# Kernel optimization log

Measured on AMD Instinct MI355X. Metric: run time of the kernel, lower is better.

Reference implementation:

```python
import jax, jax.numpy as jnp
import numpy as np

Q, C, T = 256, 128, 128
L = Q + C + T            # 512
D = 1024                 # d_model
H = 8                    # heads
DK = D // H              # 128 = self_attn.d_k
F = 3                    # num_latent_relations
R = 50                   # num_relation_kinds = len(relations2id)
FF = 4 * D               # feed-forward hidden
DEFAULT_QQ_ID = 0        # relations2id['q:q-default']
EPS = 1e-5


def setup_inputs():
    key = jax.random.key(0)
    ks = jax.random.split(key, 40)
    s = 0.02
    def nrm(k, shape, scale=s):
        return jax.random.normal(k, shape, jnp.float32) * scale
    inp = {
        'x': jax.random.normal(ks[0], (1, L, D), jnp.float32),
        'qc_relation': jax.random.uniform(ks[1], (Q, C, F), jnp.float32),
        'cq_relation': jax.random.uniform(ks[2], (C, Q, F), jnp.float32),
        'qt_relation': jax.random.uniform(ks[3], (Q, T, F), jnp.float32),
        'tq_relation': jax.random.uniform(ks[4], (T, Q, F), jnp.float32),
        'ct_relation': jax.random.randint(ks[5], (C + T, C + T), 0, R, jnp.int32),
        'predefined_relation': jax.random.randint(ks[6], (L, L), 0, R, jnp.int32),
        'mask': jnp.ones((1, L, L), jnp.int32),
        # relation embedding tables
        'rel_k_emb': nrm(ks[7], (R, DK)), 'rel_v_emb': nrm(ks[8], (R, DK)),
        'lqc_k': nrm(ks[9], (F, DK)), 'lqc_v': nrm(ks[10], (F, DK)),
        'lcq_k': nrm(ks[11], (F, DK)), 'lcq_v': nrm(ks[12], (F, DK)),
        'lqt_k': nrm(ks[13], (F, DK)), 'lqt_v': nrm(ks[14], (F, DK)),
        'ltq_k': nrm(ks[15], (F, DK)), 'ltq_v': nrm(ks[16], (F, DK)),
        # attention projections (torch Linear: y = x @ W.T + b)
        'Wq': nrm(ks[17], (D, D)), 'bq': jnp.zeros((D,), jnp.float32),
        'Wk': nrm(ks[18], (D, D)), 'bk': jnp.zeros((D,), jnp.float32),
        'Wv': nrm(ks[19], (D, D)), 'bv': jnp.zeros((D,), jnp.float32),
        'Wo': nrm(ks[20], (D, D)), 'bo': jnp.zeros((D,), jnp.float32),
        # layer norms
        'ln1_g': jnp.ones((D,), jnp.float32), 'ln1_b': jnp.zeros((D,), jnp.float32),
        'ln2_g': jnp.ones((D,), jnp.float32), 'ln2_b': jnp.zeros((D,), jnp.float32),
        # FFN
        'W1': nrm(ks[21], (FF, D)), 'b1': jnp.zeros((FF,), jnp.float32),
        'W2': nrm(ks[22], (D, FF)), 'b2': jnp.zeros((D,), jnp.float32),
    }
    return inp


def layer_norm(x, g, b):
    m = jnp.mean(x, -1, keepdims=True)
    v = jnp.mean((x - m) ** 2, -1, keepdims=True)
    return (x - m) * jax.lax.rsqrt(v + EPS) * g + b


def build_latent_relation(ct, qc, cq, qt, tq, emb, lqc, lcq, lqt, ltq):
    # qq block: every entry is the default-qq embedding row
    qq = jnp.broadcast_to(emb[DEFAULT_QQ_ID], (Q, Q, DK))
    qc_e = jnp.einsum('qcf,fd->qcd', qc, lqc)
    cq_e = jnp.einsum('cqf,fd->cqd', cq, lcq)
    qt_e = jnp.einsum('qtf,fd->qtd', qt, lqt)
    tq_e = jnp.einsum('tqf,fd->tqd', tq, ltq)
    ct_e = emb[ct]                                      # [(c+t),(c+t),DK]
    top = jnp.concatenate([qq, qc_e, qt_e], axis=1)      # [Q, L, DK]
    bot = jnp.concatenate([jnp.concatenate([cq_e, tq_e], 0), ct_e], axis=1)  # [C+T, L, DK]
    return jnp.concatenate([top, bot], axis=0)           # [L, L, DK]


def relation_attention(x, rel_k, rel_v, mask, Wq, bq, Wk, bk, Wv, bv, Wo, bo):
    B = x.shape[0]
    def proj(W, b):
        return (x @ W.T + b).reshape(B, L, H, DK).transpose(0, 2, 1, 3)  # [B,H,L,DK]
    q, k, v = proj(Wq, bq), proj(Wk, bk), proj(Wv, bv)
    scores = (jnp.einsum('bhid,bhjd->bhij', q, k)
              + jnp.einsum('bhid,ijd->bhij', q, rel_k)) / jnp.sqrt(jnp.float32(DK))
    scores = jnp.where(mask[:, None] == 0, jnp.float32(-1e9), scores)
    p = jax.nn.softmax(scores, axis=-1)
    o = (jnp.einsum('bhij,bhjd->bhid', p, v)
         + jnp.einsum('bhij,ijd->bhid', p, rel_v))
    o = o.transpose(0, 2, 1, 3).reshape(B, L, D)
    return o @ Wo.T + bo


def reference(x, qc_relation, cq_relation, qt_relation, tq_relation,
              ct_relation, predefined_relation, mask,
              rel_k_emb, rel_v_emb, lqc_k, lqc_v, lcq_k, lcq_v,
              lqt_k, lqt_v, ltq_k, ltq_v,
              Wq, bq, Wk, bk, Wv, bv, Wo, bo,
              ln1_g, ln1_b, ln2_g, ln2_b, W1, b1, W2, b2):
    # latent relation build + combine with predefined lookup
    rel_k = (rel_k_emb[predefined_relation]
             + build_latent_relation(ct_relation, qc_relation, cq_relation,
                                     qt_relation, tq_relation,
                                     rel_k_emb, lqc_k, lcq_k, lqt_k, ltq_k))
    rel_v = (rel_v_emb[predefined_relation]
             + build_latent_relation(ct_relation, qc_relation, cq_relation,
                                     qt_relation, tq_relation,
                                     rel_v_emb, lqc_v, lcq_v, lqt_v, ltq_v))
    # sublayer 0: pre-norm relation-biased self attention (dropout=0)
    h = x + relation_attention(layer_norm(x, ln1_g, ln1_b), rel_k, rel_v, mask,
                               Wq, bq, Wk, bk, Wv, bv, Wo, bo)
    # sublayer 1: pre-norm FFN
    y = layer_norm(h, ln2_g, ln2_b)
    ffn = jax.nn.relu(y @ W1.T + b1) @ W2.T + b2
    return h + ffn
```

## Files before the change

### kernel.cpp

```cpp
#include <hip/hip_runtime.h>
#include <hip/hip_bf16.h>

#define LL 512
#define DD 1024
#define HH 8
#define DKK 128
#define QQ 256
#define CCC 128
#define TTT 128
#define RR 50
#define FFF 4096
#define KLD 576
#define SLD 576

typedef __attribute__((ext_vector_type(8))) short short8;
typedef __attribute__((ext_vector_type(4))) float float4v;

__device__ __forceinline__ unsigned short f2bu(float f) {
  __hip_bfloat16 h = __float2bfloat16(f);
  unsigned short u; __builtin_memcpy(&u, &h, 2); return u;
}
__device__ __forceinline__ float b2f(unsigned short u) {
  unsigned int v = ((unsigned int)u) << 16;
  float f; __builtin_memcpy(&f, &v, 4); return f;
}
__device__ __forceinline__ int4 cvt8(float4 x, float4 y) {
  int4 o;
  o.x = (int)f2bu(x.x) | ((int)f2bu(x.y) << 16);
  o.y = (int)f2bu(x.z) | ((int)f2bu(x.w) << 16);
  o.z = (int)f2bu(y.x) | ((int)f2bu(y.y) << 16);
  o.w = (int)f2bu(y.z) | ((int)f2bu(y.w) << 16);
  return o;
}

__device__ __forceinline__ void lds_barrier() {
  __builtin_amdgcn_sched_barrier(0);
  __builtin_amdgcn_s_waitcnt(0xC07F);
  __builtin_amdgcn_s_barrier();
  __builtin_amdgcn_sched_barrier(0);
}

#define LOADSET(A0,A1,B0,B1,F0,F1,F2,F3,itv) { int k0v = (itv) << 6;          \
  A0 = *(const int4*)(Az + (size_t)(bm + r)*lda + k0v + gc*8);                \
  A1 = *(const int4*)(Az + (size_t)(bm + 32 + r)*lda + k0v + gc*8);           \
  if constexpr (!CONVB) {                                                     \
    B0 = *(const int4*)(Bz16 + (size_t)(bnb + r)*ldb + k0v + gc*8);           \
    if constexpr (NB > 1)                                                     \
      B1 = *(const int4*)(Bz16 + (size_t)(bnb + 32 + r)*ldb + k0v + gc*8);    \
  } else {                                                                    \
    F0 = *(const float4*)(Bz32 + (size_t)(bnb + r)*ldb + k0v + gc*8);         \
    F1 = *(const float4*)(Bz32 + (size_t)(bnb + r)*ldb + k0v + gc*8 + 4);     \
    if constexpr (NB > 1) {                                                   \
      F2 = *(const float4*)(Bz32 + (size_t)(bnb + 32 + r)*ldb + k0v + gc*8);  \
      F3 = *(const float4*)(Bz32 + (size_t)(bnb + 32 + r)*ldb + k0v + gc*8 + 4); } } }

#define STORESET2(basep,A0,A1,B0,B1,F0,F1,F2,F3) {                            \
  char* bse = (basep);                                                        \
  *(int4*)(bse + r*128 + sl*16) = A0;                                         \
  *(int4*)(bse + (32 + r)*128 + sl*16) = A1;                                  \
  if constexpr (!CONVB) {                                                     \
    *(int4*)(bse + ABYTES + r*128 + sl*16) = B0;                              \
    if constexpr (NB > 1)                                                     \
      *(int4*)(bse + ABYTES + (32 + r)*128 + sl*16) = B1;                     \
  } else {                                                                    \
    *(int4*)(bse + ABYTES + r*128 + sl*16) = cvt8(F0, F1);                    \
    if constexpr (NB > 1)                                                     \
      *(int4*)(bse + ABYTES + (32 + r)*128 + sl*16) = cvt8(F2, F3); } }

__global__ __launch_bounds__(256) void kprep_kernel(
    const float* __restrict__ embk,
    const float* __restrict__ lqc, const float* __restrict__ lqt,
    const float* __restrict__ lcq, const float* __restrict__ ltq,
    unsigned short* __restrict__ Kh)
{
  int g = blockIdx.x*256 + threadIdx.x;
  if (g >= 8*64*128) return;
  int d = g & 127, rr = (g >> 7) & 63, h = g >> 13;
  float v = 0.f;
  if (rr < 50) v = embk[rr*128 + d];
  else if (rr < 62) {
    int u = rr - 50; int tb = u/3, f = u - tb*3;
    const float* tab = (tb==0) ? lqc : (tb==1) ? lqt : (tb==2) ? lcq : ltq;
    v = tab[f*128 + d];
  }
  Kh[((size_t)h*KLD + 512 + rr)*DKK + d] = f2bu(v);
}

__global__ __launch_bounds__(256) void ln_bf16_kernel(const float* __restrict__ x,
    const float* __restrict__ g, const float* __restrict__ b,
    unsigned short* __restrict__ y)
{
  int row = blockIdx.x, t = threadIdx.x;
  const float4 xv = ((const float4*)(x + row*DD))[t];
  float s  = xv.x+xv.y+xv.z+xv.w;
  float ss = xv.x*xv.x+xv.y*xv.y+xv.z*xv.z+xv.w*xv.w;
  __shared__ float rs[256], rss[256];
  rs[t]=s; rss[t]=ss; __syncthreads();
  for (int st=128; st>0; st>>=1){ if (t<st){ rs[t]+=rs[t+st]; rss[t]+=rss[t+st]; } __syncthreads(); }
  float mean = rs[0] * (1.0f/DD);
  float var  = rss[0]*(1.0f/DD) - mean*mean;
  float inv  = rsqrtf(var + 1e-5f);
  float4 gv = ((const float4*)g)[t], bv = ((const float4*)b)[t];
  ushort4 ov;
  ov.x = f2bu((xv.x-mean)*inv*gv.x + bv.x);
  ov.y = f2bu((xv.y-mean)*inv*gv.y + bv.y);
  ov.z = f2bu((xv.z-mean)*inv*gv.z + bv.z);
  ov.w = f2bu((xv.w-mean)*inv*gv.w + bv.w);
  ((ushort4*)(y + row*DD))[t] = ov;
}

__global__ __launch_bounds__(256) void ln_bf16_addb_kernel(float* __restrict__ x,
    const float* __restrict__ g, const float* __restrict__ b,
    const float* __restrict__ b2, unsigned short* __restrict__ y)
{
  int row = blockIdx.x, t = threadIdx.x;
  const float4 xv = ((const float4*)(x + row*DD))[t];
  float s  = xv.x+xv.y+xv.z+xv.w;
  float ss = xv.x*xv.x+xv.y*xv.y+xv.z*xv.z+xv.w*xv.w;
  __shared__ float rs[256], rss[256];
  rs[t]=s; rss[t]=ss; __syncthreads();
  for (int st=128; st>0; st>>=1){ if (t<st){ rs[t]+=rs[t+st]; rss[t]+=rss[t+st]; } __syncthreads(); }
  float mean = rs[0] * (1.0f/DD);
  float var  = rss[0]*(1.0f/DD) - mean*mean;
  float inv  = rsqrtf(var + 1e-5f);
  float4 gv = ((const float4*)g)[t], bv = ((const float4*)b)[t];
  ushort4 ov;
  ov.x = f2bu((xv.x-mean)*inv*gv.x + bv.x);
  ov.y = f2bu((xv.y-mean)*inv*gv.y + bv.y);
  ov.z = f2bu((xv.z-mean)*inv*gv.z + bv.z);
  ov.w = f2bu((xv.w-mean)*inv*gv.w + bv.w);
  ((ushort4*)(y + row*DD))[t] = ov;
  float4 b2v = ((const float4*)b2)[t];
  float4 nx; nx.x = xv.x+b2v.x; nx.y = xv.y+b2v.y; nx.z = xv.z+b2v.z; nx.w = xv.w+b2v.w;
  ((float4*)(x + row*DD))[t] = nx;
}

template<int BN, int DEPTH, int CONVB, int ZK, int OUT_BF16, int RELU, int HAS_SRC, int HAS_BIAS>
__global__ __launch_bounds__(256) void gemm_pl(
    const unsigned short* __restrict__ A, int lda, size_t sAz,
    const void* __restrict__ Bv, int ldb, size_t sBz,
    const float* __restrict__ bias,
    const float* __restrict__ src, int ldsrc, size_t sSz,
    void* __restrict__ Cv, int ldc, size_t sCz,
    int K)
{
  constexpr int BM = 64;
  constexpr int WM = 32, WN = BN/2, FM = 2, FN = WN/16;
  constexpr int NB = BN/32;
  constexpr int ABYTES = BM*128, TILE = ABYTES + BN*128;
  __shared__ char lds[2*TILE];
  int t = threadIdx.x, w = t >> 6, l = t & 63;
  size_t z = blockIdx.z;
  const unsigned short* Az = A + z*sAz;
  const unsigned short* Bz16 = (const unsigned short*)Bv + (CONVB ? 0 : z*sBz);
  const float*          Bz32 = (const float*)Bv + (CONVB ? z*sBz : 0);
  int bm = blockIdx.y*BM, bn = blockIdx.x*BN;
  int bnb = bn;
  int wm = (w>>1)*WM, wn = (w&1)*WN;

  float4v acc[FM][FN];
  #pragma unroll
  for (int m=0;m<FM;++m)
    #pragma unroll
    for (int n=0;n<FN;++n) acc[m][n] = (float4v){0.f,0.f,0.f,0.f};

  int r = t >> 3, sl = t & 7;
  int gc = sl ^ (r & 7);
  int quad = l >> 4, lrow = l & 15;
  const int nit = K >> 6;

  int4 Aa0, Aa1, Ab0, Ab1;  float4 Af0, Af1, Af2, Af3;
  int4 Ba0, Ba1, Bb0, Bb1;  float4 Bf0, Bf1, Bf2, Bf3;
  int4 Ca0, Ca1, Cb0, Cb1;  float4 Cf0, Cf1, Cf2, Cf3;
  int4 Da0, Da1, Db0, Db1;  float4 Df0, Df1, Df2, Df3;

  auto compute = [&](const char* base) {
    const char* ab = base;
    const char* bb = base + ABYTES;
    #pragma unroll
    for (int step=0; step<2; ++step) {
      int c = step*4 + quad;
      short8 af[FM], bf[FN];
      #pragma unroll
      for (int m=0;m<FM;++m) {
        int Rw = wm + m*16 + lrow;
        af[m] = *(const short8*)(ab + Rw*128 + ((c ^ (Rw & 7))*16));
      }
      #pragma unroll
      for (int n=0;n<FN;++n) {
        int Rw = wn + n*16 + lrow;
        bf[n] = *(const short8*)(bb + Rw*128 + ((c ^ (Rw & 7))*16));
      }
      #pragma unroll
      for (int m=0;m<FM;++m)
        #pragma unroll
        for (int n=0;n<FN;++n)
          acc[m][n] = __builtin_amdgcn_mfma_f32_16x16x32_bf16(af[m], bf[n], acc[m][n], 0, 0, 0);
    }
  };

  if constexpr (DEPTH == 2) {
    LOADSET(Aa0,Aa1,Ab0,Ab1,Af0,Af1,Af2,Af3, 0);
    LOADSET(Ba0,Ba1,Bb0,Bb1,Bf0,Bf1,Bf2,Bf3, 1);
    for (int it = 0; it < nit; it += 2) {
      STORESET2(lds, Aa0,Aa1,Ab0,Ab1,Af0,Af1,Af2,Af3);
      if (it + 2 < nit) LOADSET(Aa0,Aa1,Ab0,Ab1,Af0,Af1,Af2,Af3, it+2);
      lds_barrier();
      compute(lds);
      STORESET2(lds + TILE, Ba0,Ba1,Bb0,Bb1,Bf0,Bf1,Bf2,Bf3);
      if (it + 3 < nit) LOADSET(Ba0,Ba1,Bb0,Bb1,Bf0,Bf1,Bf2,Bf3, it+3);
      lds_barrier();
      compute(lds + TILE);
    }
  } else {
    LOADSET(Aa0,Aa1,Ab0,Ab1,Af0,Af1,Af2,Af3, 0);
    LOADSET(Ba0,Ba1,Bb0,Bb1,Bf0,Bf1,Bf2,Bf3, 1);
    LOADSET(Ca0,Ca1,Cb0,Cb1,Cf0,Cf1,Cf2,Cf3, 2);
    LOADSET(Da0,Da1,Db0,Db1,Df0,Df1,Df2,Df3, 3);
    for (int it = 0; it < nit; it += 4) {
      STORESET2(lds, Aa0,Aa1,Ab0,Ab1,Af0,Af1,Af2,Af3);
      if (it + 4 < nit) LOADSET(Aa0,Aa1,Ab0,Ab1,Af0,Af1,Af2,Af3, it+4);
      lds_barrier();
      compute(lds);
      STORESET2(lds + TILE, Ba0,Ba1,Bb0,Bb1,Bf0,Bf1,Bf2,Bf3);
      if (it + 5 < nit) LOADSET(Ba0,Ba1,Bb0,Bb1,Bf0,Bf1,Bf2,Bf3, it+5);
      lds_barrier();
      compute(lds + TILE);
      STORESET2(lds, Ca0,Ca1,Cb0,Cb1,Cf0,Cf1,Cf2,Cf3);
      if (it + 6 < nit) LOADSET(Ca0,Ca1,Cb0,Cb1,Cf0,Cf1,Cf2,Cf3, it+6);
      lds_barrier();
      compute(lds);
      STORESET2(lds + TILE, Da0,Da1,Db0,Db1,Df0,Df1,Df2,Df3);
      if (it + 7 < nit) LOADSET(Da0,Da1,Db0,Db1,Df0,Df1,Df2,Df3, it+7);
      lds_barrier();
      compute(lds + TILE);
    }
  }

  #pragma unroll
  for (int m=0;m<FM;++m)
    #pragma unroll
    for (int n=0;n<FN;++n)
      #pragma unroll
      for (int rg=0;rg<4;++rg) {
        int row = bm + wm + m*16 + quad*4 + rg;
        int col = bn + wn + n*16 + lrow;
        float vv = acc[m][n][rg];
        if (ZK) {
          atomicAdd(&((float*)Cv)[(size_t)row*ldc + col], vv);
        } else {
          if (HAS_BIAS) vv += bias[col];
          if (HAS_SRC)  vv += src[z*sSz + (size_t)row*ldsrc + col];
          if (RELU) vv = fmaxf(vv, 0.f);
          if (OUT_BF16) ((unsigned short*)Cv)[z*sCz + (size_t)row*ldc + col] = f2bu(vv);
          else          ((float*)Cv)[z*sCz + (size_t)row*ldc + col] = vv;
        }
      }
}

__global__ __launch_bounds__(256) void gemm_qkv_pl(
    const unsigned short* __restrict__ A,
    const float* __restrict__ Wq, const float* __restrict__ Wk,
    const float* __restrict__ Wv,
    const float* __restrict__ bq, const float* __restrict__ bk,
    const float* __restrict__ bv,
    unsigned short* __restrict__ Qh, unsigned short* __restrict__ Kh,
    unsigned short* __restrict__ Vt)
{
  constexpr int BN = 64, CONVB = 1;
  constexpr int WM = 32, WN = 32, FM = 2, FN = 2;
  constexpr int NB = 2;
  constexpr int ABYTES = 64*128, TILE = ABYTES + BN*128;
  __shared__ char lds[2*TILE];
  int t = threadIdx.x, w = t >> 6, l = t & 63;
  int bm = blockIdx.y*64, bn = blockIdx.x*BN;
  int wm = (w>>1)*WM, wn = (w&1)*WN;
  const int lda = DD, ldb = DD, nit = DD >> 6;
  const unsigned short* Az = A;
  int part0 = bn >> 10;
  const float* Bz32 = (part0==0 ? Wq : part0==1 ? Wk : Wv) + (size_t)(bn & 1023)*DD;
  const unsigned short* Bz16 = nullptr; (void)Bz16;
  int bnb = 0;

  float4v acc[FM][FN];
  #pragma unroll
  for (int m=0;m<FM;++m)
    #pragma unroll
    for (int n=0;n<FN;++n) acc[m][n] = (float4v){0.f,0.f,0.f,0.f};

  int r = t >> 3, sl = t & 7;
  int gc = sl ^ (r & 7);
  int quad = l >> 4, lrow = l & 15;

  int4 Aa0, Aa1, Ab0, Ab1;  float4 Af0, Af1, Af2, Af3;
  int4 Ba0, Ba1, Bb0, Bb1;  float4 Bf0, Bf1, Bf2, Bf3;
  int4 Ca0, Ca1, Cb0, Cb1;  float4 Cf0, Cf1, Cf2, Cf3;
  int4 Da0, Da1, Db0, Db1;  float4 Df0, Df1, Df2, Df3;

  auto compute = [&](const char* base) {
    const char* ab = base;
    const char* bb = base + ABYTES;
    #pragma unroll
    for (int step=0; step<2; ++step) {
      int c = step*4 + quad;
      short8 af[FM], bf[FN];
      #pragma unroll
      for (int m=0;m<FM;++m) {
        int Rw = wm + m*16 + lrow;
        af[m] = *(const short8*)(ab + Rw*128 + ((c ^ (Rw & 7))*16));
      }
      #pragma unroll
      for (int n=0;n<FN;++n) {
        int Rw = wn + n*16 + lrow;
        bf[n] = *(const short8*)(bb + Rw*128 + ((c ^ (Rw & 7))*16));
      }
      #pragma unroll
      for (int m=0;m<FM;++m)
        #pragma unroll
        for (int n=0;n<FN;++n)
          acc[m][n] = __builtin_amdgcn_mfma_f32_16x16x32_bf16(af[m], bf[n], acc[m][n], 0, 0, 0);
    }
  };

  LOADSET(Aa0,Aa1,Ab0,Ab1,Af0,Af1,Af2,Af3, 0);
  LOADSET(Ba0,Ba1,Bb0,Bb1,Bf0,Bf1,Bf2,Bf3, 1);
  LOADSET(Ca0,Ca1,Cb0,Cb1,Cf0,Cf1,Cf2,Cf3, 2);
  LOADSET(Da0,Da1,Db0,Db1,Df0,Df1,Df2,Df3, 3);
  for (int it = 0; it < nit; it += 4) {
    STORESET2(lds, Aa0,Aa1,Ab0,Ab1,Af0,Af1,Af2,Af3);
    if (it + 4 < nit) LOADSET(Aa0,Aa1,Ab0,Ab1,Af0,Af1,Af2,Af3, it+4);
    lds_barrier();
    compute(lds);
    STORESET2(lds + TILE, Ba0,Ba1,Bb0,Bb1,Bf0,Bf1,Bf2,Bf3);
    if (it + 5 < nit) LOADSET(Ba0,Ba1,Bb0,Bb1,Bf0,Bf1,Bf2,Bf3, it+5);
    lds_barrier();
    compute(lds + TILE);
    STORESET2(lds, Ca0,Ca1,Cb0,Cb1,Cf0,Cf1,Cf2,Cf3);
    if (it + 6 < nit) LOADSET(Ca0,Ca1,Cb0,Cb1,Cf0,Cf1,Cf2,Cf3, it+6);
    lds_barrier();
    compute(lds);
    STORESET2(lds + TILE, Da0,Da1,Db0,Db1,Df0,Df1,Df2,Df3);
    if (it + 7 < nit) LOADSET(Da0,Da1,Db0,Db1,Df0,Df1,Df2,Df3, it+7);
    lds_barrier();
    compute(lds + TILE);
  }

  #pragma unroll
  for (int m=0;m<FM;++m)
    #pragma unroll
    for (int n=0;n<FN;++n)
      #pragma unroll
      for (int rg=0;rg<4;++rg) {
        int row = bm + wm + m*16 + quad*4 + rg;
        int col = bn + wn + n*16 + lrow;
        int part = col >> 10, hh = (col >> 7) & 7, d = col & 127;
        const float* bp = (part==0) ? bq : (part==1) ? bk : bv;
        float vv = acc[m][n][rg] + bp[col & 1023];
        unsigned short o = f2bu(vv);
        if (part == 0)      Qh[((size_t)hh*LL + row)*DKK + d] = o;
        else if (part == 1) Kh[((size_t)hh*KLD + row)*DKK + d] = o;
        else                Vt[((size_t)hh*DKK + d)*LL + row] = o;
      }
}

#define AT_QROWB 272
#define AT_KROWB 272
#define AT_SROW  584
#define AT_PROWB 1040
#define AT_VROWB 144
#define AT_OFF_KT 4352
#define AT_OFF_S  21760
#define AT_OFF_V  21760
#define AT_OFF_PW 59136
#define AT_OFF_PF1 62464
#define AT_OFF_PF2 62720
#define AT_LDS 62976

__global__ __launch_bounds__(256) void attn_fused(
    const unsigned short* __restrict__ Qh, const unsigned short* __restrict__ Kh,
    const unsigned short* __restrict__ Vt,
    const float* __restrict__ qcr, const float* __restrict__ cqr,
    const float* __restrict__ qtr, const float* __restrict__ tqr,
    const int* __restrict__ ct, const int* __restrict__ pred,
    const int* __restrict__ mask,
    const float* __restrict__ embv, const float* __restrict__ lqc_v,
    const float* __restrict__ lcq_v, const float* __restrict__ lqt_v,
    const float* __restrict__ ltq_v,
    unsigned short* __restrict__ obuf)
{
  __shared__ __align__(16) char lds[AT_LDS];
  const int t = threadIdx.x;
  const int w = t >> 6, l = t & 63, quad = l >> 4, lrow = l & 15;
  const int i0 = blockIdx.x * 16, h = blockIdx.y;

  for (int k2 = t; k2 < 960; k2 += 256) ((float*)(lds + AT_OFF_PW))[k2] = 0.f;

  {
    int qr = t >> 4, qc = t & 15;
    *(int4*)(lds + qr*AT_QROWB + qc*16) =
        *(const int4*)(Qh + ((size_t)h*LL + i0 + qr)*DKK + qc*8);
  }

  const int kr = t >> 4, kc = t & 15;
  int4 kv0, kv1, kv2, kv3;
#define AT_LOADK(jtv) { size_t kb = (size_t)h*KLD + (size_t)(jtv)*64 + kr;     \
    kv0 = *(const int4*)(Kh + (kb     )*DKK + kc*8);                           \
    kv1 = *(const int4*)(Kh + (kb + 16)*DKK + kc*8);                           \
    kv2 = *(const int4*)(Kh + (kb + 32)*DKK + kc*8);                           \
    kv3 = *(const int4*)(Kh + (kb + 48)*DKK + kc*8); }
#define AT_STOREK() {                                                          \
    *(int4*)(lds + AT_OFF_KT + (kr     )*AT_KROWB + kc*16) = kv0;              \
    *(int4*)(lds + AT_OFF_KT + (kr + 16)*AT_KROWB + kc*16) = kv1;              \
    *(int4*)(lds + AT_OFF_KT + (kr + 32)*AT_KROWB + kc*16) = kv2;              \
    *(int4*)(lds + AT_OFF_KT + (kr + 48)*AT_KROWB + kc*16) = kv3; }

  AT_LOADK(0);
  for (int jt = 0; jt < 9; ++jt) {
    lds_barrier();
    AT_STOREK();
    if (jt + 1 < 9) AT_LOADK(jt + 1);
    lds_barrier();
    float4v acc = (float4v){0.f,0.f,0.f,0.f};
    #pragma unroll
    for (int kk = 0; kk < 4; ++kk) {
      int c = kk*4 + quad;
      short8 af = *(const short8*)(lds + lrow*AT_QROWB + c*16);
      short8 bf = *(const short8*)(lds + AT_OFF_KT + (w*16 + lrow)*AT_KROWB + c*16);
      acc = __builtin_amdgcn_mfma_f32_16x16x32_bf16(af, bf, acc, 0, 0, 0);
    }
    #pragma unroll
    for (int rg = 0; rg < 4; ++rg)
      ((float*)(lds + AT_OFF_S))[(quad*4 + rg)*AT_SROW + jt*64 + w*16 + lrow] = acc[rg];
  }
  lds_barrier();

  const int row = t >> 4, l16 = t & 15;
  const int i = i0 + row;
  const float* Srow = (const float*)(lds + AT_OFF_S) + row*AT_SROW;
  const int base = (i0 < QQ) ? 562 : (i0 < QQ + CCC) ? 568 : 571;
  const float lq1a = Srow[base], lq1b = Srow[base+1], lq1c = Srow[base+2];
  const float lq2a = Srow[565], lq2b = Srow[566], lq2c = Srow[567];

  const int vr = t >> 3, vc = t & 7;
  int4 vv0, vv1, vv2, vv3;
#define AT_LOADV(itv) { size_t vb = (size_t)h*DKK + vr;                        \
    size_t vo = (size_t)(itv)*64 + vc*8;                                       \
    vv0 = *(const int4*)(Vt + (vb      )*LL + vo);                             \
    vv1 = *(const int4*)(Vt + (vb + 32)*LL + vo);                              \
    vv2 = *(const int4*)(Vt + (vb + 64)*LL + vo);                              \
    vv3 = *(const int4*)(Vt + (vb + 96)*LL + vo); }
#define AT_STOREV() {                                                          \
    *(int4*)(lds + AT_OFF_V + (vr     )*AT_VROWB + vc*16) = vv0;               \
    *(int4*)(lds + AT_OFF_V + (vr + 32)*AT_VROWB + vc*16) = vv1;               \
    *(int4*)(lds + AT_OFF_V + (vr + 64)*AT_VROWB + vc*16) = vv2;               \
    *(int4*)(lds + AT_OFF_V + (vr + 96)*AT_VROWB + vc*16) = vv3; }
  AT_LOADV(0);

  float sv[32];
  #pragma unroll
  for (int m = 0; m < 32; ++m) {
    int j = m*16 + l16;
    int predv = pred[i*LL + j];
    int maskv = mask[i*LL + j];
    float s = Srow[j] + Srow[512 + predv];
    if (i0 < QQ) {
      if (j < QQ) s += Srow[512];
      else if (j < QQ + CCC) {
        const float* r3 = qcr + ((size_t)i*CCC + (j - QQ))*3;
        s += r3[0]*lq1a + r3[1]*lq1b + r3[2]*lq1c;
      } else {
        const float* r3 = qtr + ((size_t)i*TTT + (j - QQ - CCC))*3;
        s += r3[0]*lq2a + r3[1]*lq2b + r3[2]*lq2c;
      }
    } else {
      if (j < QQ) {
        const float* r3 = (i < QQ + CCC) ? cqr + ((size_t)(i - QQ)*QQ + j)*3
                                         : tqr + ((size_t)(i - QQ - CCC)*QQ + j)*3;
        s += r3[0]*lq1a + r3[1]*lq1b + r3[2]*lq1c;
      } else {
        int scat2 = ct[(i - QQ)*(CCC + TTT) + (j - QQ)];
        s += Srow[512 + scat2];
      }
    }
    s *= 0.08838834764831845f;
    if (maskv == 0) s = -1e9f;
    sv[m] = s;
  }
  float mx = sv[0];
  #pragma unroll
  for (int m = 1; m < 32; ++m) mx = fmaxf(mx, sv[m]);
  #pragma unroll
  for (int off = 8; off >= 1; off >>= 1) mx = fmaxf(mx, __shfl_xor(mx, off));
  float sum = 0.f;
  #pragma unroll
  for (int m = 0; m < 32; ++m) { float e = __expf(sv[m] - mx); sv[m] = e; sum += e; }
  #pragma unroll
  for (int off = 8; off >= 1; off >>= 1) sum += __shfl_xor(sum, off);
  const float inv = 1.0f / sum;

  float f0=0.f, f1=0.f, f2=0.f, g0=0.f, g1=0.f, g2=0.f;
  #pragma unroll
  for (int m = 0; m < 32; ++m) {
    int j = m*16 + l16;
    float p = sv[m] * inv;
    *(unsigned short*)(lds + row*AT_PROWB + j*2) = f2bu(p);
    int predv = pred[i*LL + j];
    atomicAdd((float*)(lds + AT_OFF_PW) + row*52 + predv, p);
    if (i0 < QQ) {
      if (j < QQ) atomicAdd((float*)(lds + AT_OFF_PW) + row*52, p);
      else if (j < QQ + CCC) {
        const float* r3 = qcr + ((size_t)i*CCC + (j - QQ))*3;
        f0 += p*r3[0]; f1 += p*r3[1]; f2 += p*r3[2];
      } else {
        const float* r3 = qtr + ((size_t)i*TTT + (j - QQ - CCC))*3;
        g0 += p*r3[0]; g1 += p*r3[1]; g2 += p*r3[2];
      }
    } else {
      if (j < QQ) {
        const float* r3 = (i < QQ + CCC) ? cqr + ((size_t)(i - QQ)*QQ + j)*3
                                         : tqr + ((size_t)(i - QQ - CCC)*QQ + j)*3;
        f0 += p*r3[0]; f1 += p*r3[1]; f2 += p*r3[2];
      } else {
        int scat2 = ct[(i - QQ)*(CCC + TTT) + (j - QQ)];
        atomicAdd((float*)(lds + AT_OFF_PW) + row*52 + scat2, p);
      }
    }
  }
  #pragma unroll
  for (int off = 8; off >= 1; off >>= 1) {
    f0 += __shfl_xor(f0, off); f1 += __shfl_xor(f1, off); f2 += __shfl_xor(f2, off);
    g0 += __shfl_xor(g0, off); g1 += __shfl_xor(g1, off); g2 += __shfl_xor(g2, off);
  }
  if (l16 == 0) {
    float* pf1 = (float*)(lds + AT_OFF_PF1) + row*4;
    float* pf2 = (float*)(lds + AT_OFF_PF2) + row*4;
    pf1[0] = f0; pf1[1] = f1; pf1[2] = f2;
    pf2[0] = g0; pf2[1] = g1; pf2[2] = g2;
  }

  float4v oacc0 = (float4v){0.f,0.f,0.f,0.f};
  float4v oacc1 = (float4v){0.f,0.f,0.f,0.f};
  for (int it = 0; it < 8; ++it) {
    lds_barrier();
    AT_STOREV();
    if (it + 1 < 8) AT_LOADV(it + 1);
    lds_barrier();
    #pragma unroll
    for (int kk = 0; kk < 2; ++kk) {
      int c = kk*4 + quad;
      short8 pa = *(const short8*)(lds + lrow*AT_PROWB + it*128 + c*16);
      short8 vf0 = *(const short8*)(lds + AT_OFF_V + (w*32 + lrow)*AT_VROWB + c*16);
      short8 vf1 = *(const short8*)(lds + AT_OFF_V + (w*32 + 16 + lrow)*AT_VROWB + c*16);
      oacc0 = __builtin_amdgcn_mfma_f32_16x16x32_bf16(pa, vf0, oacc0, 0, 0, 0);
      oacc1 = __builtin_amdgcn_mfma_f32_16x16x32_bf16(pa, vf1, oacc1, 0, 0, 0);
    }
  }

  const float* tab1 = (i0 < QQ) ? lqc_v : (i0 < QQ + CCC) ? lcq_v : ltq_v;
  const bool hasT2 = (i0 < QQ);
  const float* pws = (const float*)(lds + AT_OFF_PW);
  #pragma unroll
  for (int n = 0; n < 2; ++n) {
    int d = w*32 + n*16 + lrow;
    float a0=0.f, a1=0.f, a2=0.f, a3=0.f;
    #pragma unroll 5
    for (int rr = 0; rr < RR; ++rr) {
      float evv = embv[rr*DKK + d];
      a0 += pws[(quad*4+0)*52 + rr]*evv;
      a1 += pws[(quad*4+1)*52 + rr]*evv;
      a2 += pws[(quad*4+2)*52 + rr]*evv;
      a3 += pws[(quad*4+3)*52 + rr]*evv;
    }
    float t0 = tab1[d], t1 = tab1[DKK + d], t2 = tab1[2*DKK + d];
    float u0 = 0.f, u1 = 0.f, u2 = 0.f;
    if (hasT2) { u0 = lqt_v[d]; u1 = lqt_v[DKK + d]; u2 = lqt_v[2*DKK + d]; }
    #pragma unroll
    for (int rg = 0; rg < 4; ++rg) {
      int rw = quad*4 + rg;
      const float* pf1 = (const float*)(lds + AT_OFF_PF1) + rw*4;
      const float* pf2 = (const float*)(lds + AT_OFF_PF2) + rw*4;
      float aval = (rg==0) ? a0 : (rg==1) ? a1 : (rg==2) ? a2 : a3;
      float oval = (n==0) ? oacc0[rg] : oacc1[rg];
      float val = oval + aval
                + pf1[0]*t0 + pf1[1]*t1 + pf1[2]*t2
                + pf2[0]*u0 + pf2[1]*u1 + pf2[2]*u2;
      obuf[(size_t)(i0 + rw)*DD + h*DKK + d] = f2bu(val);
    }
  }
}

extern "C" void kernel_launch(void* const* d_in, const int* in_sizes, int n_in,
                              void* d_out, int out_size, void* d_ws, size_t ws_size,
                              hipStream_t stream)
{
  const float* x    = (const float*)d_in[0];
  const float* qcr  = (const float*)d_in[1];
  const float* cqr  = (const float*)d_in[2];
  const float* qtr  = (const float*)d_in[3];
  const float* tqr  = (const float*)d_in[4];
  const int*   ct   = (const int*)d_in[5];
  const int*   pred = (const int*)d_in[6];
  const int*   mask = (const int*)d_in[7];
  const float* embk = (const float*)d_in[8];
  const float* embv = (const float*)d_in[9];
  const float* lqc_k = (const float*)d_in[10];
  const float* lqc_v = (const float*)d_in[11];
  const float* lcq_k = (const float*)d_in[12];
  const float* lcq_v = (const float*)d_in[13];
  const float* lqt_k = (const float*)d_in[14];
  const float* lqt_v = (const float*)d_in[15];
  const float* ltq_k = (const float*)d_in[16];
  const float* ltq_v = (const float*)d_in[17];
  const float* Wq = (const float*)d_in[18]; const float* bq = (const float*)d_in[19];
  const float* Wk = (const float*)d_in[20]; const float* bk = (const float*)d_in[21];
  const float* Wv = (const float*)d_in[22]; const float* bv = (const float*)d_in[23];
  const float* Wo = (const float*)d_in[24]; const float* bo = (const float*)d_in[25];
  const float* ln1_g = (const float*)d_in[26]; const float* ln1_b = (const float*)d_in[27];
  const float* ln2_g = (const float*)d_in[28]; const float* ln2_b = (const float*)d_in[29];
  const float* W1 = (const float*)d_in[30]; const float* b1 = (const float*)d_in[31];
  const float* W2 = (const float*)d_in[32]; const float* b2 = (const float*)d_in[33];
  float* out = (float*)d_out;

  float* wsf = (float*)d_ws;
  float* S    = wsf;
  float* o2   = S + (size_t)HH*LL*SLD;
  unsigned short* ub = (unsigned short*)(o2 + (size_t)HH*LL*DKK);
  unsigned short* ybuf_b = ub;
  unsigned short* obuf_b = ybuf_b + LL*DD;
  unsigned short* Qh     = obuf_b + LL*DD;
  unsigned short* Kh     = Qh + (size_t)HH*LL*DKK;
  unsigned short* Vt     = Kh + (size_t)HH*KLD*DKK;
  unsigned short* hidden = (unsigned short*)S;

  kprep_kernel<<<(8*64*128 + 255)/256, 256, 0, stream>>>(
      embk, lqc_k, lqt_k, lcq_k, ltq_k, Kh);
  ln_bf16_kernel<<<LL, 256, 0, stream>>>(x, ln1_g, ln1_b, ybuf_b);
  gemm_qkv_pl<<<dim3(48, 8), 256, 0, stream>>>(ybuf_b, Wq, Wk, Wv, bq, bk, bv,
                                               Qh, Kh, Vt);
  attn_fused<<<dim3(32, 8), 256, 0, stream>>>(
      Qh, Kh, Vt, qcr, cqr, qtr, tqr, ct, pred, mask,
      embv, lqc_v, lcq_v, lqt_v, ltq_v, obuf_b);
  gemm_pl<32,4,1,0,0,0,1,1><<<dim3(32, 8, 1), 256, 0, stream>>>(
      obuf_b, DD, 0, Wo, DD, 0, bo, x, DD, 0, out, DD, 0, DD);
  ln_bf16_addb_kernel<<<LL, 256, 0, stream>>>(out, ln2_g, ln2_b, b2, ybuf_b);
  gemm_pl<64,4,1,0,1,1,0,1><<<dim3(64, 8, 1), 256, 0, stream>>>(
      ybuf_b, DD, 0, W1, DD, 0, b1, nullptr, 0, 0, hidden, FFF, 0, DD);
  gemm_pl<64,4,1,1,0,0,0,0><<<dim3(16, 8, 4), 256, 0, stream>>>(
      hidden, FFF, (size_t)1024, W2, FFF, (size_t)1024,
      nullptr, nullptr, 0, 0, out, DD, 0, 1024);
}
```

Measured before the change: 249.5 us.

## Halve attention query tile, double-buffer K/V, and defer softmax normalization

The fused attention kernel now handles 8 query rows per block instead of 16, so it launches twice as many blocks across heads. K and V tiles are double-buffered in LDS, which removes one barrier per step. Softmax no longer subtracts a running max: unnormalized exponentials are used directly and the whole output is scaled by 1/sum at the end, merging two passes into one. In exchange, half of each 16-row MFMA tile is wasted, and skipping the max subtraction risks overflow if scores are large.

Result: no change. 247.3 us (-0.9%).

```diff
diff --git a/kernel.cpp b/kernel.cpp
--- a/kernel.cpp
+++ b/kernel.cpp
@@ -363,18 +363,22 @@
       }
 }
 
-#define AT_QROWB 272
-#define AT_KROWB 272
-#define AT_SROW  584
-#define AT_PROWB 1040
-#define AT_VROWB 144
-#define AT_OFF_KT 4352
-#define AT_OFF_S  21760
-#define AT_OFF_V  21760
-#define AT_OFF_PW 59136
-#define AT_OFF_PF1 62464
-#define AT_OFF_PF2 62720
-#define AT_LDS 62976
+#define A2_QROWB 272
+#define A2_KROWB 272
+#define A2_SROWD 586
+#define A2_PROWB 1040
+#define A2_VROWB 136
+#define A2_OFF_KA 2176
+#define A2_OFF_KB 19584
+#define A2_OFF_S  36992
+#define A2_OFF_P  2176
+#define A2_OFF_VA 10496
+#define A2_OFF_VB 27904
+#define A2_OFF_PW 55744
+#define A2_OFF_PF1 57408
+#define A2_OFF_PF2 57536
+#define A2_OFF_SI 57664
+#define A2_LDS 57696
 
 __global__ __launch_bounds__(256) void attn_fused(
     const unsigned short* __restrict__ Qh, const unsigned short* __restrict__ Kh,
@@ -388,203 +392,213 @@
     const float* __restrict__ ltq_v,
     unsigned short* __restrict__ obuf)
 {
-  __shared__ __align__(16) char lds[AT_LDS];
+  __shared__ __align__(16) char lds[A2_LDS];
   const int t = threadIdx.x;
   const int w = t >> 6, l = t & 63, quad = l >> 4, lrow = l & 15;
-  const int i0 = blockIdx.x * 16, h = blockIdx.y;
-
-  for (int k2 = t; k2 < 960; k2 += 256) ((float*)(lds + AT_OFF_PW))[k2] = 0.f;
-
-  {
+  const int i0 = blockIdx.x * 8, h = blockIdx.y;
+
+  for (int k2 = t; k2 < 488; k2 += 256) ((float*)(lds + A2_OFF_PW))[k2] = 0.f;
+
+  if (t < 128) {
     int qr = t >> 4, qc = t & 15;
-    *(int4*)(lds + qr*AT_QROWB + qc*16) =
+    *(int4*)(lds + qr*A2_QROWB + qc*16) =
         *(const int4*)(Qh + ((size_t)h*LL + i0 + qr)*DKK + qc*8);
   }
 
   const int kr = t >> 4, kc = t & 15;
-  int4 kv0, kv1, kv2, kv3;
-#define AT_LOADK(jtv) { size_t kb = (size_t)h*KLD + (size_t)(jtv)*64 + kr;     \
-    kv0 = *(const int4*)(Kh + (kb     )*DKK + kc*8);                           \
-    kv1 = *(const int4*)(Kh + (kb + 16)*DKK + kc*8);                           \
-    kv2 = *(const int4*)(Kh + (kb + 32)*DKK + kc*8);                           \
-    kv3 = *(const int4*)(Kh + (kb + 48)*DKK + kc*8); }
-#define AT_STOREK() {                                                          \
-    *(int4*)(lds + AT_OFF_KT + (kr     )*AT_KROWB + kc*16) = kv0;              \
-    *(int4*)(lds + AT_OFF_KT + (kr + 16)*AT_KROWB + kc*16) = kv1;              \
-    *(int4*)(lds + AT_OFF_KT + (kr + 32)*AT_KROWB + kc*16) = kv2;              \
-    *(int4*)(lds + AT_OFF_KT + (kr + 48)*AT_KROWB + kc*16) = kv3; }
-
-  AT_LOADK(0);
-  for (int jt = 0; jt < 9; ++jt) {
-    lds_barrier();
-    AT_STOREK();
-    if (jt + 1 < 9) AT_LOADK(jt + 1);
-    lds_barrier();
+  int4 ka0,ka1,ka2,ka3, kb0,kb1,kb2,kb3;
+
+#define A2_LOADKA(jtv) { size_t kb_ = (size_t)h*KLD + (size_t)(jtv)*64 + kr;   \
+    ka0 = *(const int4*)(Kh + (kb_     )*DKK + kc*8);                          \
+    ka1 = *(const int4*)(Kh + (kb_ + 16)*DKK + kc*8);                          \
+    ka2 = *(const int4*)(Kh + (kb_ + 32)*DKK + kc*8);                          \
+    ka3 = *(const int4*)(Kh + (kb_ + 48)*DKK + kc*8); }
+#define A2_LOADKB(jtv) { size_t kb_ = (size_t)h*KLD + (size_t)(jtv)*64 + kr;   \
+    kb0 = *(const int4*)(Kh + (kb_     )*DKK + kc*8);                          \
+    kb1 = *(const int4*)(Kh + (kb_ + 16)*DKK + kc*8);                          \
+    kb2 = *(const int4*)(Kh + (kb_ + 32)*DKK + kc*8);                          \
+    kb3 = *(const int4*)(Kh + (kb_ + 48)*DKK + kc*8); }
+#define A2_STOREKA() { char* p_ = lds + A2_OFF_KA;                             \
+    *(int4*)(p_ + (kr     )*A2_KROWB + kc*16) = ka0;                           \
+    *(int4*)(p_ + (kr + 16)*A2_KROWB + kc*16) = ka1;                           \
+    *(int4*)(p_ + (kr + 32)*A2_KROWB + kc*16) = ka2;                           \
+    *(int4*)(p_ + (kr + 48)*A2_KROWB + kc*16) = ka3; }
+#define A2_STOREKB() { char* p_ = lds + A2_OFF_KB;                             \
+    *(int4*)(p_ + (kr     )*A2_KROWB + kc*16) = kb0;                           \
+    *(int4*)(p_ + (kr + 16)*A2_KROWB + kc*16) = kb1;                           \
+    *(int4*)(p_ + (kr + 32)*A2_KROWB + kc*16) = kb2;                           \
+    *(int4*)(p_ + (kr + 48)*A2_KROWB + kc*16) = kb3; }
+
+  auto qk_tile = [&](const char* kb, int jt) {
     float4v acc = (float4v){0.f,0.f,0.f,0.f};
     #pragma unroll
     for (int kk = 0; kk < 4; ++kk) {
       int c = kk*4 + quad;
-      short8 af = *(const short8*)(lds + lrow*AT_QROWB + c*16);
-      short8 bf = *(const short8*)(lds + AT_OFF_KT + (w*16 + lrow)*AT_KROWB + c*16);
+      short8 af = *(const short8*)(lds + lrow*A2_QROWB + c*16);
+      short8 bf = *(const short8*)(kb + (w*16 + lrow)*A2_KROWB + c*16);
       acc = __builtin_amdgcn_mfma_f32_16x16x32_bf16(af, bf, acc, 0, 0, 0);
     }
-    #pragma unroll
-    for (int rg = 0; rg < 4; ++rg)
-      ((float*)(lds + AT_OFF_S))[(quad*4 + rg)*AT_SROW + jt*64 + w*16 + lrow] = acc[rg];
-  }
+    if (quad < 2) {
+      #pragma unroll
+      for (int rg = 0; rg < 4; ++rg)
+        ((float*)(lds + A2_OFF_S))[(quad*4 + rg)*A2_SROWD + jt*64 + w*16 + lrow] = acc[rg];
+    }
+  };
+
+  A2_LOADKA(0); A2_LOADKB(1);
+  A2_STOREKA(); A2_LOADKA(2); lds_barrier(); qk_tile(lds + A2_OFF_KA, 0);
+  A2_STOREKB(); A2_LOADKB(3); lds_barrier(); qk_tile(lds + A2_OFF_KB, 1);
+  A2_STOREKA(); A2_LOADKA(4); lds_barrier(); qk_tile(lds + A2_OFF_KA, 2);
+  A2_STOREKB(); A2_LOADKB(5); lds_barrier(); qk_tile(lds + A2_OFF_KB, 3);
+  A2_STOREKA(); A2_LOADKA(6); lds_barrier(); qk_tile(lds + A2_OFF_KA, 4);
+  A2_STOREKB(); A2_LOADKB(7); lds_barrier(); qk_tile(lds + A2_OFF_KB, 5);
+  A2_STOREKA(); A2_LOADKA(8); lds_barrier(); qk_tile(lds + A2_OFF_KA, 6);
+  A2_STOREKB();               lds_barrier(); qk_tile(lds + A2_OFF_KB, 7);
+  A2_STOREKA();               lds_barrier(); qk_tile(lds + A2_OFF_KA, 8);
   lds_barrier();
 
-  const int row = t >> 4, l16 = t & 15;
+  const int row = t >> 5, l32 = t & 31;
   const int i = i0 + row;
-  const float* Srow = (const float*)(lds + AT_OFF_S) + row*AT_SROW;
-  const int base = (i0 < QQ) ? 562 : (i0 < QQ + CCC) ? 568 : 571;
-  const float lq1a = Srow[base], lq1b = Srow[base+1], lq1c = Srow[base+2];
-  const float lq2a = Srow[565], lq2b = Srow[566], lq2c = Srow[567];
+  const float* Sp = (const float*)(lds + A2_OFF_S) + row*A2_SROWD;
+  const int bse = (i0 < QQ) ? 562 : (i0 < QQ + CCC) ? 568 : 571;
+  const float lq1a = Sp[bse], lq1b = Sp[bse+1], lq1c = Sp[bse+2];
+  const float lq2a = Sp[565], lq2b = Sp[566], lq2c = Sp[567];
 
   const int vr = t >> 3, vc = t & 7;
-  int4 vv0, vv1, vv2, vv3;
-#define AT_LOADV(itv) { size_t vb = (size_t)h*DKK + vr;                        \
-    size_t vo = (size_t)(itv)*64 + vc*8;                                       \
-    vv0 = *(const int4*)(Vt + (vb      )*LL + vo);                             \
-    vv1 = *(const int4*)(Vt + (vb + 32)*LL + vo);                              \
-    vv2 = *(const int4*)(Vt + (vb + 64)*LL + vo);                              \
-    vv3 = *(const int4*)(Vt + (vb + 96)*LL + vo); }
-#define AT_STOREV() {                                                          \
-    *(int4*)(lds + AT_OFF_V + (vr     )*AT_VROWB + vc*16) = vv0;               \
-    *(int4*)(lds + AT_OFF_V + (vr + 32)*AT_VROWB + vc*16) = vv1;               \
-    *(int4*)(lds + AT_OFF_V + (vr + 64)*AT_VROWB + vc*16) = vv2;               \
-    *(int4*)(lds + AT_OFF_V + (vr + 96)*AT_VROWB + vc*16) = vv3; }
-  AT_LOADV(0);
-
-  float sv[32];
+  int4 va0,va1,va2,va3, vb0,vb1,vb2,vb3;
+#define A2_LOADVA(itv) { size_t vb_ = (size_t)h*DKK + vr;                      \
+    size_t vo_ = (size_t)(itv)*64 + vc*8;                                      \
+    va0 = *(const int4*)(Vt + (vb_      )*LL + vo_);                           \
+    va1 = *(const int4*)(Vt + (vb_ + 32)*LL + vo_);                            \
+    va2 = *(const int4*)(Vt + (vb_ + 64)*LL + vo_);                            \
+    va3 = *(const int4*)(Vt + (vb_ + 96)*LL + vo_); }
+#define A2_LOADVB(itv) { size_t vb_ = (size_t)h*DKK + vr;                      \
+    size_t vo_ = (size_t)(itv)*64 + vc*8;                                      \
+    vb0 = *(const int4*)(Vt + (vb_      )*LL + vo_);                           \
+    vb1 = *(const int4*)(Vt + (vb_ + 32)*LL + vo_);                            \
+    vb2 = *(const int4*)(Vt + (vb_ + 64)*LL + vo_);                            \
+    vb3 = *(const int4*)(Vt + (vb_ + 96)*LL + vo_); }
+#define A2_STOREVA() { char* p_ = lds + A2_OFF_VA;                             \
+    *(int4*)(p_ + (vr     )*A2_VROWB + vc*16) = va0;                           \
+    *(int4*)(p_ + (vr + 32)*A2_VROWB + vc*16) = va1;                           \
+    *(int4*)(p_ + (vr + 64)*A2_VROWB + vc*16) = va2;                           \
+    *(int4*)(p_ + (vr + 96)*A2_VROWB + vc*16) = va3; }
+#define A2_STOREVB() { char* p_ = lds + A2_OFF_VB;                             \
+    *(int4*)(p_ + (vr     )*A2_VROWB + vc*16) = vb0;                           \
+    *(int4*)(p_ + (vr + 32)*A2_VROWB + vc*16) = vb1;                           \
+    *(int4*)(p_ + (vr + 64)*A2_VROWB + vc*16) = vb2;                           \
+    *(int4*)(p_ + (vr + 96)*A2_VROWB + vc*16) = vb3; }
+
+  A2_LOADVA(0); A2_LOADVB(1);
+
+  float sum=0.f, f0=0.f, f1=0.f, f2=0.f, g0=0.f, g1=0.f, g2=0.f;
+  float* pwsrow = (float*)(lds + A2_OFF_PW) + row*52;
   #pragma unroll
-  for (int m = 0; m < 32; ++m) {
-    int j = m*16 + l16;
+  for (int m = 0; m < 16; ++m) {
+    int j = m*32 + l32;
     int predv = pred[i*LL + j];
     int maskv = mask[i*LL + j];
-    float s = Srow[j] + Srow[512 + predv];
+    float s = Sp[j] + Sp[512 + predv];
+    float c0=0.f, c1=0.f, c2=0.f; int rt; int scat2 = 0;
     if (i0 < QQ) {
-      if (j < QQ) s += Srow[512];
+      if (j < QQ) { s += Sp[512]; rt = 0; }
       else if (j < QQ + CCC) {
         const float* r3 = qcr + ((size_t)i*CCC + (j - QQ))*3;
-        s += r3[0]*lq1a + r3[1]*lq1b + r3[2]*lq1c;
+        c0 = r3[0]; c1 = r3[1]; c2 = r3[2];
+        s += c0*lq1a + c1*lq1b + c2*lq1c; rt = 1;
       } else {
         const float* r3 = qtr + ((size_t)i*TTT + (j - QQ - CCC))*3;
-        s += r3[0]*lq2a + r3[1]*lq2b + r3[2]*lq2c;
+        c0 = r3[0]; c1 = r3[1]; c2 = r3[2];
+        s += c0*lq2a + c1*lq2b + c2*lq2c; rt = 2;
       }
     } else {
       if (j < QQ) {
         const float* r3 = (i < QQ + CCC) ? cqr + ((size_t)(i - QQ)*QQ + j)*3
                                          : tqr + ((size_t)(i - QQ - CCC)*QQ + j)*3;
-        s += r3[0]*lq1a + r3[1]*lq1b + r3[2]*lq1c;
+        c0 = r3[0]; c1 = r3[1]; c2 = r3[2];
+        s += c0*lq1a + c1*lq1b + c2*lq1c; rt = 1;
       } else {
-        int scat2 = ct[(i - QQ)*(CCC + TTT) + (j - QQ)];
-        s += Srow[512 + scat2];
+        scat2 = ct[(i - QQ)*(CCC + TTT) + (j - QQ)];
+        s += Sp[512 + scat2]; rt = 0;
       }
     }
     s *= 0.08838834764831845f;
-    if (maskv == 0) s = -1e9f;
-    sv[m] = s;
-  }
-  float mx = sv[0];
+    float e = (maskv == 0) ? 0.f : __expf(s);
+    sum += e;
+    *(unsigned short*)(lds + A2_OFF_P + row*A2_PROWB + j*2) = f2bu(e);
+    atomicAdd(pwsrow + predv, e);
+    if (rt == 0)      atomicAdd(pwsrow + scat2, e);
+    else if (rt == 1) { f0 += e*c0; f1 += e*c1; f2 += e*c2; }
+    else              { g0 += e*c0; g1 += e*c1; g2 += e*c2; }
+  }
   #pragma unroll
-  for (int m = 1; m < 32; ++m) mx = fmaxf(mx, sv[m]);
-  #pragma unroll
-  for (int off = 8; off >= 1; off >>= 1) mx = fmaxf(mx, __shfl_xor(mx, off));
-  float sum = 0.f;
-  #pragma unroll
-  for (int m = 0; m < 32; ++m) { float e = __expf(sv[m] - mx); sv[m] = e; sum += e; }
-  #pragma unroll
-  for (int off = 8; off >= 1; off >>= 1) sum += __shfl_xor(sum, off);
-  const float inv = 1.0f / sum;
-
-  float f0=0.f, f1=0.f, f2=0.f, g0=0.f, g1=0.f, g2=0.f;
-  #pragma unroll
-  for (int m = 0; m < 32; ++m) {
-    int j = m*16 + l16;
-    float p = sv[m] * inv;
-    *(unsigned short*)(lds + row*AT_PROWB + j*2) = f2bu(p);
-    int predv = pred[i*LL + j];
-    atomicAdd((float*)(lds + AT_OFF_PW) + row*52 + predv, p);
-    if (i0 < QQ) {
-      if (j < QQ) atomicAdd((float*)(lds + AT_OFF_PW) + row*52, p);
-      else if (j < QQ + CCC) {
-        const float* r3 = qcr + ((size_t)i*CCC + (j - QQ))*3;
-        f0 += p*r3[0]; f1 += p*r3[1]; f2 += p*r3[2];
-      } else {
-        const float* r3 = qtr + ((size_t)i*TTT + (j - QQ - CCC))*3;
-        g0 += p*r3[0]; g1 += p*r3[1]; g2 += p*r3[2];
-      }
-    } else {
-      if (j < QQ) {
-        const float* r3 = (i < QQ + CCC) ? cqr + ((size_t)(i - QQ)*QQ + j)*3
-                                         : tqr + ((size_t)(i - QQ - CCC)*QQ + j)*3;
-        f0 += p*r3[0]; f1 += p*r3[1]; f2 += p*r3[2];
-      } else {
-        int scat2 = ct[(i - QQ)*(CCC + TTT) + (j - QQ)];
-        atomicAdd((float*)(lds + AT_OFF_PW) + row*52 + scat2, p);
-      }
-    }
-  }
-  #pragma unroll
-  for (int off = 8; off >= 1; off >>= 1) {
+  for (int off = 16; off >= 1; off >>= 1) {
+    sum += __shfl_xor(sum, off);
     f0 += __shfl_xor(f0, off); f1 += __shfl_xor(f1, off); f2 += __shfl_xor(f2, off);
     g0 += __shfl_xor(g0, off); g1 += __shfl_xor(g1, off); g2 += __shfl_xor(g2, off);
   }
-  if (l16 == 0) {
-    float* pf1 = (float*)(lds + AT_OFF_PF1) + row*4;
-    float* pf2 = (float*)(lds + AT_OFF_PF2) + row*4;
+  if (l32 == 0) {
+    float* pf1 = (float*)(lds + A2_OFF_PF1) + row*4;
+    float* pf2 = (float*)(lds + A2_OFF_PF2) + row*4;
     pf1[0] = f0; pf1[1] = f1; pf1[2] = f2;
     pf2[0] = g0; pf2[1] = g1; pf2[2] = g2;
+    ((float*)(lds + A2_OFF_SI))[row] = 1.0f / sum;
   }
 
   float4v oacc0 = (float4v){0.f,0.f,0.f,0.f};
   float4v oacc1 = (float4v){0.f,0.f,0.f,0.f};
-  for (int it = 0; it < 8; ++it) {
-    lds_barrier();
-    AT_STOREV();
-    if (it + 1 < 8) AT_LOADV(it + 1);
-    lds_barrier();
+  auto pv_tile = [&](const char* vbase, int it) {
     #pragma unroll
     for (int kk = 0; kk < 2; ++kk) {
       int c = kk*4 + quad;
-      short8 pa = *(const short8*)(lds + lrow*AT_PROWB + it*128 + c*16);
-      short8 vf0 = *(const short8*)(lds + AT_OFF_V + (w*32 + lrow)*AT_VROWB + c*16);
-      short8 vf1 = *(const short8*)(lds + AT_OFF_V + (w*32 + 16 + lrow)*AT_VROWB + c*16);
+      short8 pa  = *(const short8*)(lds + A2_OFF_P + lrow*A2_PROWB + it*128 + c*16);
+      short8 vf0 = *(const short8*)(vbase + (w*32 + lrow)*A2_VROWB + c*16);
+      short8 vf1 = *(const short8*)(vbase + (w*32 + 16 + lrow)*A2_VROWB + c*16);
       oacc0 = __builtin_amdgcn_mfma_f32_16x16x32_bf16(pa, vf0, oacc0, 0, 0, 0);
       oacc1 = __builtin_amdgcn_mfma_f32_16x16x32_bf16(pa, vf1, oacc1, 0, 0, 0);
     }
-  }
-
-  const float* tab1 = (i0 < QQ) ? lqc_v : (i0 < QQ + CCC) ? lcq_v : ltq_v;
-  const bool hasT2 = (i0 < QQ);
-  const float* pws = (const float*)(lds + AT_OFF_PW);
-  #pragma unroll
-  for (int n = 0; n < 2; ++n) {
-    int d = w*32 + n*16 + lrow;
-    float a0=0.f, a1=0.f, a2=0.f, a3=0.f;
-    #pragma unroll 5
-    for (int rr = 0; rr < RR; ++rr) {
-      float evv = embv[rr*DKK + d];
-      a0 += pws[(quad*4+0)*52 + rr]*evv;
-      a1 += pws[(quad*4+1)*52 + rr]*evv;
-      a2 += pws[(quad*4+2)*52 + rr]*evv;
-      a3 += pws[(quad*4+3)*52 + rr]*evv;
-    }
-    float t0 = tab1[d], t1 = tab1[DKK + d], t2 = tab1[2*DKK + d];
-    float u0 = 0.f, u1 = 0.f, u2 = 0.f;
-    if (hasT2) { u0 = lqt_v[d]; u1 = lqt_v[DKK + d]; u2 = lqt_v[2*DKK + d]; }
-    #pragma unroll
-    for (int rg = 0; rg < 4; ++rg) {
-      int rw = quad*4 + rg;
-      const float* pf1 = (const float*)(lds + AT_OFF_PF1) + rw*4;
-      const float* pf2 = (const float*)(lds + AT_OFF_PF2) + rw*4;
-      float aval = (rg==0) ? a0 : (rg==1) ? a1 : (rg==2) ? a2 : a3;
-      float oval = (n==0) ? oacc0[rg] : oacc1[rg];
-      float val = oval + aval
-                + pf1[0]*t0 + pf1[1]*t1 + pf1[2]*t2
-                + pf2[0]*u0 + pf2[1]*u1 + pf2[2]*u2;
-      obuf[(size_t)(i0 + rw)*DD + h*DKK + d] = f2bu(val);
+  };
+  A2_STOREVA(); A2_LOADVA(2); lds_barrier(); pv_tile(lds + A2_OFF_VA, 0);
+  A2_STOREVB(); A2_LOADVB(3); lds_barrier(); pv_tile(lds + A2_OFF_VB, 1);
+  A2_STOREVA(); A2_LOADVA(4); lds_barrier(); pv_tile(lds + A2_OFF_VA, 2);
+  A2_STOREVB(); A2_LOADVB(5); lds_barrier(); pv_tile(lds + A2_OFF_VB, 3);
+  A2_STOREVA(); A2_LOADVA(6); lds_barrier(); pv_tile(lds + A2_OFF_VA, 4);
+  A2_STOREVB(); A2_LOADVB(7); lds_barrier(); pv_tile(lds + A2_OFF_VB, 5);
+  A2_STOREVA();               lds_barrier(); pv_tile(lds + A2_OFF_VA, 6);
+  A2_STOREVB();               lds_barrier(); pv_tile(lds + A2_OFF_VB, 7);
+
+  if (quad < 2) {
+    const float* tab1 = (i0 < QQ) ? lqc_v : (i0 < QQ + CCC) ? lcq_v : ltq_v;
+    const bool hasT2 = (i0 < QQ);
+    const float* pws = (const float*)(lds + A2_OFF_PW);
+    const float* sinv = (const float*)(lds + A2_OFF_SI);
+    #pragma unroll
+    for (int n = 0; n < 2; ++n) {
+      int d = w*32 + n*16 + lrow;
+      float a0=0.f, a1=0.f, a2=0.f, a3=0.f;
+      #pragma unroll 5
+      for (int rr = 0; rr < RR; ++rr) {
+        float evv = embv[rr*DKK + d];
+        a0 += pws[(quad*4+0)*52 + rr]*evv;
+        a1 += pws[(quad*4+1)*52 + rr]*evv;
+        a2 += pws[(quad*4+2)*52 + rr]*evv;
+        a3 += pws[(quad*4+3)*52 + rr]*evv;
+      }
+      float t0 = tab1[d], t1 = tab1[DKK + d], t2 = tab1[2*DKK + d];
+      float u0 = 0.f, u1 = 0.f, u2 = 0.f;
+      if (hasT2) { u0 = lqt_v[d]; u1 = lqt_v[DKK + d]; u2 = lqt_v[2*DKK + d]; }
+      #pragma unroll
+      for (int rg = 0; rg < 4; ++rg) {
+        int rw = quad*4 + rg;
+        const float* pf1 = (const float*)(lds + A2_OFF_PF1) + rw*4;
+        const float* pf2 = (const float*)(lds + A2_OFF_PF2) + rw*4;
+        float aval = (rg==0) ? a0 : (rg==1) ? a1 : (rg==2) ? a2 : a3;
+        float oval = (n==0) ? oacc0[rg] : oacc1[rg];
+        float val = (oval + aval
+                  + pf1[0]*t0 + pf1[1]*t1 + pf1[2]*t2
+                  + pf2[0]*u0 + pf2[1]*u1 + pf2[2]*u2) * sinv[rw];
+        obuf[(size_t)(i0 + rw)*DD + h*DKK + d] = f2bu(val);
+      }
     }
   }
 }
@@ -637,7 +651,7 @@
   ln_bf16_kernel<<<LL, 256, 0, stream>>>(x, ln1_g, ln1_b, ybuf_b);
   gemm_qkv_pl<<<dim3(48, 8), 256, 0, stream>>>(ybuf_b, Wq, Wk, Wv, bq, bk, bv,
                                                Qh, Kh, Vt);
-  attn_fused<<<dim3(32, 8), 256, 0, stream>>>(
+  attn_fused<<<dim3(64, 8), 256, 0, stream>>>(
       Qh, Kh, Vt, qcr, cqr, qtr, tqr, ct, pred, mask,
       embv, lqc_v, lcq_v, lqt_v, ltq_v, obuf_b);
   gemm_pl<32,4,1,0,0,0,1,1><<<dim3(32, 8, 1), 256, 0, stream>>>(
```
